# Performance work log

Measured on AMD Instinct MI355X. Metric: run time of the kernel, lower is better.

## Reference

```python
import jax, jax.numpy as jnp
import numpy as np

B, S, V, E, H, L = 32, 64, 96, 256, 512, 3
DIN = 2 * H  # padded input width for stacked LSTM weight tensors


def _cell(x, h, c, Wih, Whh, bih, bhh):
    # PyTorch LSTMCell gate order: i, f, g, o
    g = x @ Wih.T + h @ Whh.T + bih + bhh
    i, f, gg, o = jnp.split(g, 4, axis=-1)
    c2 = jax.nn.sigmoid(f) * c + jax.nn.sigmoid(i) * jnp.tanh(gg)
    h2 = jax.nn.sigmoid(o) * jnp.tanh(c2)
    return h2, c2


def _pad_feat(x, d):
    p = d - x.shape[-1]
    return x if p == 0 else jnp.pad(x, ((0, 0),) * (x.ndim - 1) + ((0, p),))


def _run_lstm(xs, Wih, Whh, bih, bhh, reverse):
    # xs: [S, B, Din]
    if reverse:
        xs = xs[::-1]
    b = xs.shape[1]
    init = (jnp.zeros((b, H), xs.dtype), jnp.zeros((b, H), xs.dtype))

    def step(carry, xt):
        h, c = _cell(xt, carry[0], carry[1], Wih, Whh, bih, bhh)
        return (h, c), h

    (h, c), ys = jax.lax.scan(step, init, xs)
    if reverse:
        ys = ys[::-1]
    return ys, h, c


def setup_inputs():
    key = jax.random.key(0)
    ks = jax.random.split(key, 20)
    f = lambda k, shp, s=0.08: jax.random.normal(k, shp, jnp.float32) * s
    return {
        "src": jax.random.randint(ks[0], (B, S), 0, V - 1),  # avoids padding_idx=95
        "trg": jax.random.randint(ks[1], (B, S), 0, V - 1),
        "embedding": f(ks[2], (V, E), 0.5),
        "enc_Wih": f(ks[3], (L, 2, 4 * H, DIN)),
        "enc_Whh": f(ks[4], (L, 2, 4 * H, H)),
        "enc_bih": f(ks[5], (L, 2, 4 * H)),
        "enc_bhh": f(ks[6], (L, 2, 4 * H)),
        "dec_Wih": f(ks[7], (L, 4 * H, DIN)),
        "dec_Whh": f(ks[8], (L, 4 * H, H)),
        "dec_bih": f(ks[9], (L, 4 * H)),
        "dec_bhh": f(ks[10], (L, 4 * H)),
        "attn_W": f(ks[11], (H, 3 * H)),
        "attn_b": f(ks[12], (H,)),
        "attn_v": jax.random.uniform(ks[13], (H,), jnp.float32),
        "proj_W": f(ks[14], (2 * H, E + 2 * H)),
        "proj_b": f(ks[15], (2 * H,)),
        "fc_W": f(ks[16], (V, H)),
        "fc_b": f(ks[17], (V,)),
    }


def _forward(src, trg, embedding, enc_Wih, enc_Whh, enc_bih, enc_bhh,
             dec_Wih, dec_Whh, dec_bih, dec_bhh, attn_W, attn_b, attn_v,
             proj_W, proj_b, fc_W, fc_b):
    emb = embedding[src]                 # [B,S,E]; dropout=identity (eval)
    xs = emb.transpose(1, 0, 2)          # [S,B,E]
    h_sum, c_sum = [], []
    for l in range(L):
        xin = _pad_feat(xs, DIN)         # zero-pad so stacked weights apply; padded cols hit zeros
        yf, hf, cf = _run_lstm(xin, enc_Wih[l, 0], enc_Whh[l, 0], enc_bih[l, 0], enc_bhh[l, 0], False)
        yb, hb, cb = _run_lstm(xin, enc_Wih[l, 1], enc_Whh[l, 1], enc_bih[l, 1], enc_bhh[l, 1], True)
        xs = jnp.concatenate([yf, yb], -1)  # [S,B,2H]
        h_sum.append(hf + hb)
        c_sum.append(cf + cb)            # hidden.view(L,2,B,H).sum(dim=1)
    enc_out = xs.transpose(1, 0, 2)      # [B,S,2H]
    dec_h, dec_c = jnp.stack(h_sum), jnp.stack(c_sum)  # [L,B,H]

    tokens = trg[:, :-1].T               # teacher_forcing_ratio = 1.0 (deterministic)

    def dec_step(carry, tok):
        h, c = carry
        htop = h[-1]                     # [B,H]
        rep = jnp.concatenate([jnp.broadcast_to(htop[:, None, :], (B, S, H)), enc_out], -1)
        energy = jnp.tanh(rep @ attn_W.T + attn_b)               # [B,S,H]
        attn = jax.nn.softmax(jnp.einsum('d,bsd->bs', attn_v, energy), axis=1)
        context = jnp.einsum('bs,bsd->bd', attn, enc_out)        # [B,2H]
        x = jnp.concatenate([embedding[tok], context], -1) @ proj_W.T + proj_b  # [B,2H]
        hs, cs = [], []
        xin = x
        for l in range(L):
            hl, cl = _cell(_pad_feat(xin, DIN), h[l], c[l], dec_Wih[l], dec_Whh[l], dec_bih[l], dec_bhh[l])
            hs.append(hl)
            cs.append(cl)
            xin = hl
        out = xin @ fc_W.T + fc_b        # [B,V]
        return (jnp.stack(hs), jnp.stack(cs)), out

    _, outs = jax.lax.scan(dec_step, (dec_h, dec_c), tokens)     # [S-1,B,V]
    outputs = jnp.concatenate([jnp.zeros((1, B, V), outs.dtype), outs], 0)
    return outputs.transpose(1, 0, 2)    # [B,S,V]; t=0 row is zeros, matching torch


def reference(src, trg, embedding, enc_Wih, enc_Whh, enc_bih, enc_bhh,
              dec_Wih, dec_Whh, dec_bih, dec_bhh, attn_W, attn_b, attn_v,
              proj_W, proj_b, fc_W, fc_b):
    return _forward(src, trg, embedding, enc_Wih, enc_Whh, enc_bih, enc_bhh,
                    dec_Wih, dec_Whh, dec_bih, dec_bhh, attn_W, attn_b, attn_v,
                    proj_W, proj_b, fc_W, fc_b)
```

## Files before the change

### kernel.cpp

```cpp
#include <hip/hip_runtime.h>

#define B_ 32
#define S_ 64
#define V_ 96
#define E_ 256
#define H_ 512
#define L_ 3
#define DIN_ 1024
#define G4_ 2048
#define BH_ (B_*H_)
#define BDIN_ (B_*DIN_)
#define FSTRIDE 16

typedef unsigned short u16;

__device__ __forceinline__ float bfu(u16 u){ return __uint_as_float(((unsigned)u) << 16); }
__device__ __forceinline__ u16 f2b(float f){
  unsigned x = __float_as_uint(f);
  unsigned r = (x + 0x7FFFu + ((x >> 16) & 1u)) >> 16;
  return (u16)r;
}
__device__ __forceinline__ float sigm(float x){ return 1.f/(1.f+__expf(-x)); }
__device__ __forceinline__ float bsum(float a){
  #pragma unroll
// ... 201 lines not shown
    const int bE = lane & 31;
    const float* Gp = a.G + (size_t)(t*B_+bE)*4096 + (size_t)d*G4_ + j;
    float pg0=Gp[0], pg1=Gp[512], pg2=Gp[1024], pg3=Gp[1536];

    float gv0=0.f, gv1=0.f, gv2=0.f, gv3=0.f;
    for(int b=half*16; b<half*16+16; b++){
      float gs[4] = {0.f,0.f,0.f,0.f};
      const float* hp = &SM[(b<<9) + (lane<<2)];
      #pragma unroll
      for(int pp=0;pp<2;pp++){
        float4 hv = *(const float4*)(hp + pp*256);
        float ha[4] = {hv.x,hv.y,hv.z,hv.w};
        #pragma unroll
        for(int gg=0;gg<4;gg++){
          #pragma unroll
          for(int i=0;i<4;i++) gs[gg] = fmaf(ha[i], wh[gg][pp*4+i], gs[gg]);
        }
      }
      #pragma unroll
      for(int gg=0;gg<4;gg++) gs[gg] = bsum(gs[gg]);
      if(lane == b){ gv0=gs[0]; gv1=gs[1]; gv2=gs[2]; gv3=gs[3]; }
    }
    if(own){
      float gi = gv0+pg0, gf = gv1+pg1, gG = gv2+pg2, go = gv3+pg3;
      float c2 = sigm(gf)*cv + sigm(gi)*tanhf(gG);
      float h2 = sigm(go)*tanhf(c2);
      cv = c2;
      stc(&a.henc[(size_t)(((p+1)&63)*2 + d)*BH_ + (size_t)lane*H_ + j], h2);
      a.Xout[(size_t)(t*B_+lane)*DIN_ + (d<<9) + j] = h2;
    }
    gbar(a.flags, ++g);
  }
  if(own) stc(&a.cT[ci], cv);
  gbar(a.flags, ++g);
  for(int i = blockIdx.x*512 + tid; i < BH_; i += 131072){
    float hf2 = a.henc[(size_t)(0*2+0)*BH_ + i];
    float hb2 = a.henc[(size_t)(0*2+1)*BH_ + i];
    a.dh0[(size_t)a.l*BH_ + i] = hf2 + hb2;
    a.dcT[(size_t)a.l*BH_ + i] = ldc(&a.cT[i]) + ldc(&a.cT[BH_ + i]);
  }
}
__global__ __launch_bounds__(512,1) void k_enc2(EncArgs2 a){
  if(*a.fl) enc2_body<1>(a); else enc2_body<0>(a);
}

struct DecArgs2 {
  const int* trg;
  const void* emb; const void* aW; const void* av; const void* pW; const void* pb;
  const void* dWih; const void* dWhh; const void* dbih; const void* dbhh;
  const void* fW; const void* fb;
  const float* Epre; const float* X3;
  const float* dh0;
  float* dhb;
  float* zb;
  u16*   ctxb;
  float* xpb;
  const float* dcT;
  void* out;
  const int* fl;
  int* flags; int gbase;
};

template<int BF, int CP>
__device__ __forceinline__ void dec2_cell(const DecArgs2& a, float* SM,
    const int t, const int l, const int jp, const int bh, const int bh_blk,
    const int lane, const int tid, const int half, int& g, float& cv){
  constexpr int Kx  = CP*256;
  constexpr int HB  = (CP==4) ? 2 : 1;
  constexpr int NBs = 16/HB;
  constexpr int NW  = NBs/2;
  const float* xsrc = (l==0) ? (a.xpb + (size_t)t*BDIN_ + (size_t)bh_blk*16*DIN_)
                             : (a.dhb + (size_t)((t+1)*3 + (l-1))*BH_ + (size_t)bh_blk*16*H_);
  const float* hsrc = (t==0) ? (a.dh0 + (size_t)l*BH_ + (size_t)bh_blk*16*H_)
                             : (a.dhb + (size_t)(t*3 + l)*BH_ + (size_t)bh_blk*16*H_);
  float wx[4][CP*4];
  float wh[4][8];
  #pragma unroll
  for(int gg=0; gg<4; gg++){
    size_t rowx = ((size_t)l*G4_ + (size_t)gg*H_ + jp)*DIN_;
    #pragma unroll
    for(int p=0;p<CP;p++){
      float4 v = LD4<BF>(a.dWih, rowx + (lane<<2) + p*256);
      wx[gg][p*4+0]=v.x; wx[gg][p*4+1]=v.y; wx[gg][p*4+2]=v.z; wx[gg][p*4+3]=v.w;
    }
    size_t rowh = ((size_t)l*G4_ + (size_t)gg*H_ + jp)*H_;
    #pragma unroll
    for(int p=0;p<2;p++){
      float4 v = LD4<BF>(a.dWhh, rowh + (lane<<2) + p*256);
      wh[gg][p*4+0]=v.x; wh[gg][p*4+1]=v.y; wh[gg][p*4+2]=v.z; wh[gg][p*4+3]=v.w;
    }
  }
  float pg[4];
  {
    size_t bb = (size_t)l*G4_ + jp;
    #pragma unroll
    for(int gg=0;gg<4;gg++)
      pg[gg] = LD<BF>(a.dbih, bb + (size_t)gg*H_) + LD<BF>(a.dbhh, bb + (size_t)gg*H_);
  }
  float gv0=0.f,gv1=0.f,gv2=0.f,gv3=0.f;
  #pragma unroll
  for(int hf=0; hf<HB; hf++){
    const float* xg = xsrc + (size_t)hf*NBs*Kx;
    const float* hg = hsrc + (size_t)hf*NBs*H_;
    for(int i=tid<<2; i<NBs*Kx; i+=2048) *(float4*)&SM[i] = *(const float4*)&xg[i];
    for(int i=tid<<2; i<NBs*H_; i+=2048) *(float4*)&SM[NBs*Kx + i] = *(const float4*)&hg[i];
    __syncthreads();
    for(int ib2=half*NW; ib2<half*NW+NW; ib2++){
      const int ib = hf*NBs + ib2;
      float gs[4] = {0.f,0.f,0.f,0.f};
      const float* xr = &SM[ib2*Kx + (lane<<2)];
      #pragma unroll
      for(int p=0;p<CP;p++){
        float4 xv = *(const float4*)(xr + p*256);
        float xa[4] = {xv.x,xv.y,xv.z,xv.w};
        #pragma unroll
        for(int gg=0;gg<4;gg++){
          #pragma unroll
          for(int i=0;i<4;i++) gs[gg] = fmaf(xa[i], wx[gg][p*4+i], gs[gg]);
        }
      }
      const float* hr = &SM[NBs*Kx + ib2*H_ + (lane<<2)];
      #pragma unroll
      for(int p=0;p<2;p++){
        float4 hv = *(const float4*)(hr + p*256);
        float ha[4] = {hv.x,hv.y,hv.z,hv.w};
        #pragma unroll
        for(int gg=0;gg<4;gg++){
          #pragma unroll
          for(int i=0;i<4;i++) gs[gg] = fmaf(ha[i], wh[gg][p*4+i], gs[gg]);
        }
      }
      #pragma unroll
      for(int gg=0;gg<4;gg++) gs[gg] = bsum(gs[gg]);
      if(lane == ib){ gv0=gs[0]; gv1=gs[1]; gv2=gs[2]; gv3=gs[3]; }
    }
    __syncthreads();
  }
  const bool own = (lane < 16) && (((CP==4) ? ((lane>>2)&1) : (lane>>3)) == half);
  if(own){
    const int b = bh*16 + lane;
    float gi = gv0+pg[0], gf = gv1+pg[1], gG = gv2+pg[2], go = gv3+pg[3];
    float c2 = sigm(gf)*cv + sigm(gi)*tanhf(gG);
    float h2 = sigm(go)*tanhf(c2);
    cv = c2;
    stc(&a.dhb[(size_t)((t+1)*3 + l)*BH_ + (size_t)b*H_ + jp], h2);
  }
  gbar(a.flags, ++g);
}

template<int BF>
__device__ void dec2_body(const DecArgs2& a){
  __shared__ float SM[16384];
  const int tid  = threadIdx.x;
  const int lane = tid & 63;
  const int wid  = tid >> 6;
  const int w4   = (blockIdx.x<<2) + (wid & 3);
  const int jp   = w4 & 511;
  const int bh   = w4 >> 9;
  const int half = wid >> 2;
  const int bh_blk = blockIdx.x >> 7;
  int g = a.gbase;

  float cvs[3];
  #pragma unroll
  for(int l=0;l<3;l++)
    cvs[l] = a.dcT[((size_t)l*H_ + jp)*32 + (size_t)bh*16 + (lane&15)];

  for(int t=0; t<64; ++t){
    {
      const float* hs = (t==0) ? (a.dh0 + (size_t)2*BH_ + (size_t)bh_blk*16*H_)
                               : (a.dhb + (size_t)(t*3 + 2)*BH_ + (size_t)bh_blk*16*H_);
      for(int i=tid<<2; i<16*H_; i+=2048) *(float4*)&SM[i] = *(const float4*)&hs[i];
      __syncthreads();
      if(t < 63){
        float wz[8];
        size_t rz = (size_t)jp*1536;
        #pragma unroll
        for(int p=0;p<2;p++){
          float4 v = LD4<BF>(a.aW, rz + (lane<<2) + p*256);
          wz[p*4+0]=v.x; wz[p*4+1]=v.y; wz[p*4+2]=v.z; wz[p*4+3]=v.w;
        }
        for(int ib=half*8; ib<half*8+8; ib++){
          const float* hp = &SM[(ib<<9) + (lane<<2)];
          float acc = 0.f;
          #pragma unroll
          for(int p=0;p<2;p++){
            float4 hv = *(const float4*)(hp + p*256);
            acc = fmaf(hv.x, wz[p*4+0], acc); acc = fmaf(hv.y, wz[p*4+1], acc);
            acc = fmaf(hv.z, wz[p*4+2], acc); acc = fmaf(hv.w, wz[p*4+3], acc);
          }
          acc = bsum(acc);
          if(lane==0) stc(&a.zb[(size_t)t*BH_ + (size_t)(bh*16+ib)*H_ + jp], acc);
        }
      }
      if(t > 0){
        #pragma unroll
        for(int r=0;r<3;r++){
          const int q  = jp + (r<<9);
          const int v_ = q % 96;
          const int ib = q / 96;
          if((ib>>3) != half) continue;
          float wf[8];
          size_t rf = (size_t)v_*H_;
          #pragma unroll
          for(int p=0;p<2;p++){
            float4 v = LD4<BF>(a.fW, rf + (lane<<2) + p*256);
            wf[p*4+0]=v.x; wf[p*4+1]=v.y; wf[p*4+2]=v.z; wf[p*4+3]=v.w;
          }
          const float* hp = &SM[(ib<<9) + (lane<<2)];
          float acc = 0.f;
          #pragma unroll
          for(int p=0;p<2;p++){
            float4 hv = *(const float4*)(hp + p*256);
            acc = fmaf(hv.x, wf[p*4+0], acc); acc = fmaf(hv.y, wf[p*4+1], acc);
            acc = fmaf(hv.z, wf[p*4+2], acc); acc = fmaf(hv.w, wf[p*4+3], acc);
          }
          acc = bsum(acc);
          if(lane==0){
            float rr = acc + LD<BF>(a.fb, v_);
            size_t oi = (size_t)(bh*16+ib)*(S_*V_) + (size_t)t*V_ + v_;
            if constexpr(BF) ((u16*)a.out)[oi] = f2b(rr);
            else             ((float*)a.out)[oi] = rr;
          }
        }
      }
    }
    if(t == 63) break;
    gbar(a.flags, ++g);

    if(blockIdx.x < 32){
      const int b = blockIdx.x;
      float* Zs = SM; float* Ss = SM + 512;
      for(int i=tid; i<512; i+=512) Zs[i] = a.zb[(size_t)t*BH_ + (size_t)b*H_ + i];
      __syncthreads();
      float wa[8];
      #pragma unroll
      for(int p=0;p<2;p++){
        float4 v = LD4<BF>(a.av, (lane<<2) + p*256);
        wa[p*4+0]=v.x; wa[p*4+1]=v.y; wa[p*4+2]=v.z; wa[p*4+3]=v.w;
      }
      for(int s=wid; s<64; s+=8){
        const float* ep = a.Epre + ((size_t)(s*B_ + b))*H_;
        float acc = 0.f;
        #pragma unroll
        for(int p=0;p<2;p++){
          const float4 e4 = *(const float4*)(ep + (lane<<2) + p*256);
          const float4 z4 = *(const float4*)(Zs + (lane<<2) + p*256);
          acc = fmaf(wa[p*4+0], tanhf(e4.x+z4.x), acc);
          acc = fmaf(wa[p*4+1], tanhf(e4.y+z4.y), acc);
          acc = fmaf(wa[p*4+2], tanhf(e4.z+z4.z), acc);
          acc = fmaf(wa[p*4+3], tanhf(e4.w+z4.w), acc);
        }
        acc = bsum(acc);
        if(lane==0) Ss[s] = acc;
      }
      __syncthreads();
      if(tid < 64){
        float vv = Ss[tid];
        float m = vv;
        #pragma unroll
        for(int off=1; off<64; off<<=1) m = fmaxf(m, __shfl_xor(m, off));
        float e = __expf(vv - m);
        float su = e;
        #pragma unroll
        for(int off=1; off<64; off<<=1) su += __shfl_xor(su, off);
        Ss[tid] = e / su;
      }
      __syncthreads();
      for(int d4 = tid<<2; d4 < DIN_; d4 += 2048){
        float a0=0.f,a1=0.f,a2=0.f,a3=0.f;
        const float* xb = a.X3 + (size_t)b*DIN_ + d4;
        for(int s=0;s<64;s++){
          const float pp = Ss[s];
          const float4 xv = *(const float4*)(xb + (size_t)s*BDIN_);
          a0 = fmaf(pp, xv.x, a0); a1 = fmaf(pp, xv.y, a1);
          a2 = fmaf(pp, xv.z, a2); a3 = fmaf(pp, xv.w, a3);
        }
        u16* cp = a.ctxb + (size_t)t*BDIN_ + (size_t)b*DIN_ + d4;
        unsigned lo = (unsigned)f2b(a0) | ((unsigned)f2b(a1)<<16);
        unsigned hi = (unsigned)f2b(a2) | ((unsigned)f2b(a3)<<16);
        stci((int*)cp, (int)lo);
        stci(((int*)cp)+1, (int)hi);
      }
    }
    gbar(a.flags, ++g);

    {
      const u16* cs = a.ctxb + (size_t)t*BDIN_ + (size_t)bh_blk*16*DIN_;
      for(int i=tid*4; i<16*DIN_; i+=2048){
        ushort4 v = *(const ushort4*)(cs + i);
        *(float4*)&SM[i] = make_float4(bfu(v.x), bfu(v.y), bfu(v.z), bfu(v.w));
      }
      __syncthreads();
      float wpe[2][4], wpc[2][16];
      #pragma unroll
      for(int jj=0;jj<2;jj++){
        size_t row = (size_t)(jp + (jj<<9))*1280;
        float4 v = LD4<BF>(a.pW, row + (lane<<2));
        wpe[jj][0]=v.x; wpe[jj][1]=v.y; wpe[jj][2]=v.z; wpe[jj][3]=v.w;
        #pragma unroll
        for(int p=0;p<4;p++){
          float4 c4 = LD4<BF>(a.pW, row + 256 + (lane<<2) + p*256);
          wpc[jj][p*4+0]=c4.x; wpc[jj][p*4+1]=c4.y; wpc[jj][p*4+2]=c4.z; wpc[jj][p*4+3]=c4.w;
        }
      }
      const float pb0 = LD<BF>(a.pb, jp);
      const float pb1 = LD<BF>(a.pb, jp+512);
      for(int ib=half*8; ib<half*8+8; ib++){
        const int b = bh*16 + ib;
        const int tok = a.trg[b*S_ + t];
        float4 ev = LD4<BF>(a.emb, (size_t)tok*E_ + (lane<<2));
        float ea[4] = {ev.x, ev.y, ev.z, ev.w};
        float s0=0.f, s1=0.f;
        #pragma unroll
        for(int i=0;i<4;i++){ s0 = fmaf(ea[i], wpe[0][i], s0); s1 = fmaf(ea[i], wpe[1][i], s1); }
        const float* cp = &SM[(ib<<10) + (lane<<2)];
        #pragma unroll
        for(int p=0;p<4;p++){
          float4 c4 = *(const float4*)(cp + p*256);
          float ca[4] = {c4.x,c4.y,c4.z,c4.w};
          #pragma unroll
          for(int i=0;i<4;i++){ s0 = fmaf(ca[i], wpc[0][p*4+i], s0); s1 = fmaf(ca[i], wpc[1][p*4+i], s1); }
        }
        s0 = bsum(s0); s1 = bsum(s1);
        if(lane==0){
          stc(&a.xpb[(size_t)t*BDIN_ + (size_t)b*DIN_ + jp],       s0 + pb0);
          stc(&a.xpb[(size_t)t*BDIN_ + (size_t)b*DIN_ + jp + 512], s1 + pb1);
        }
      }
      __syncthreads();
    }
    gbar(a.flags, ++g);

    dec2_cell<BF,4>(a, SM, t, 0, jp, bh, bh_blk, lane, tid, half, g, cvs[0]);
    dec2_cell<BF,2>(a, SM, t, 1, jp, bh, bh_blk, lane, tid, half, g, cvs[1]);
    dec2_cell<BF,2>(a, SM, t, 2, jp, bh, bh_blk, lane, tid, half, g, cvs[2]);
  }
}
__global__ __launch_bounds__(512,1) void k_dec2(DecArgs2 a){
  if(*a.fl) dec2_body<1>(a); else dec2_body<0>(a);
}

struct EncArgsO {
  const float* G;
  const float* Xin;
  const void* Wih; size_t oWi;
  const void* Whh; size_t oWh;
  const void* bih; size_t obi;
  const void* bhh; size_t obh;
  float* hst; float* cT; float* Xout; float* dh; float* dcT;
  int l; const int* fl; int* flags; int gbase;
};

template<int BF, int CP>
__device__ void encO_body(const EncArgsO& a){
  __shared__ float SM[16384];
  const int tid  = threadIdx.x;
  const int w    = (blockIdx.x<<2) + (tid>>6);
  const int lane = tid & 63;
  const int d    = w >> 9;
  const int j    = w & 511;
  int g = a.gbase;

  float wh[4][8];
  #pragma unroll
  for(int gg=0; gg<4; gg++){
    size_t rowh = a.oWh + ((size_t)d*G4_ + (size_t)gg*H_ + j)*H_;
    #pragma unroll
    for(int p=0;p<2;p++){
      float4 v = LD4<BF>(a.Whh, rowh + (lane<<2) + p*256);
      wh[gg][p*4+0]=v.x; wh[gg][p*4+1]=v.y; wh[gg][p*4+2]=v.z; wh[gg][p*4+3]=v.w;
    }
  }
  float wxf[4][CP?CP*4:1];
  float pbias[4];
  if constexpr(CP>0){
    #pragma unroll
    for(int gg=0; gg<4; gg++){
      size_t rowx = a.oWi + ((size_t)d*G4_ + (size_t)gg*H_ + j)*DIN_;
      #pragma unroll
      for(int p=0;p<CP;p++){
        float4 v = LD4<BF>(a.Wih, rowx + (lane<<2) + p*256);
        wxf[gg][p*4+0]=v.x; wxf[gg][p*4+1]=v.y; wxf[gg][p*4+2]=v.z; wxf[gg][p*4+3]=v.w;
      }
    }
    size_t bb = (size_t)d*G4_ + j;
    #pragma unroll
    for(int gg=0;gg<4;gg++)
      pbias[gg] = LD<BF>(a.bih, a.obi + bb + (size_t)gg*H_)
// ... 345 lines not shown
          stc(&a.xp[(size_t)b*DIN_ + jp + 512], s1 + pb1);
        }
      }
    }
    gbar(a.flags, ++g);
    decO_cell<BF,4>(a, SM, 0, cur, jp, bh, bh_blk, lane, tid, g, cvs[0]);
    decO_cell<BF,2>(a, SM, 1, cur, jp, bh, bh_blk, lane, tid, g, cvs[1]);
    decO_cell<BF,2>(a, SM, 2, cur, jp, bh, bh_blk, lane, tid, g, cvs[2]);
    cur ^= 1;
  }
}
__global__ __launch_bounds__(256,2) void k_dec_persO(DecArgsO a){
  if(*a.fl) decO_body<1>(a); else decO_body<0>(a);
}

extern "C" void kernel_launch(void* const* d_in, const int* in_sizes, int n_in,
                              void* d_out, int out_size, void* d_ws, size_t ws_size,
                              hipStream_t stream){
  const int* src  = (const int*)d_in[0];
  const int* trg  = (const int*)d_in[1];
  const void* emb = d_in[2];
  const void* eWih= d_in[3];
  const void* eWhh= d_in[4];
  const void* ebih= d_in[5];
  const void* ebhh= d_in[6];
  const void* dWih= d_in[7];
  const void* dWhh= d_in[8];
  const void* dbih= d_in[9];
  const void* dbhh= d_in[10];
  const void* aW  = d_in[11];
  const void* ab  = d_in[12];
  const void* av  = d_in[13];
  const void* pW  = d_in[14];
  const void* pb  = d_in[15];
  const void* fW  = d_in[16];
  const void* fb  = d_in[17];

  char* base = (char*)d_ws;
  size_t off = 0;
  auto take = [&](size_t bytes)->char*{
    char* p = base + off; off = (off + bytes + 255) & ~(size_t)255; return p;
  };

  const size_t szX  = (size_t)2048*1024*4;
  const size_t szG  = (size_t)2048*4096*4;
  const size_t szE  = (size_t)2048*512*4;
  int planA = ws_size >= (size_t)53*1024*1024;

  if(planA){
    float* X    = (float*)take(szX);
    float* Xh   = (float*)take(szX);
    float* G    = (float*)take(szG);
    float* dhb  = G;
    float* zb   = dhb + (size_t)64*3*BH_;
    float* xpb  = zb  + (size_t)63*BH_;
    u16*   ctxb = (u16*)(xpb + (size_t)63*BDIN_);
    float* Epre = (float*)take(szE);
    float* cTe  = (float*)take((size_t)2*BH_*4);
    float* dh0  = (float*)take((size_t)3*BH_*4);
    float* dcT  = (float*)take((size_t)3*BH_*4);
    int* fl     = (int*)take(256);
    int* flags  = (int*)take((256*FSTRIDE + 16)*4);

    k_detect<<<1, 256, 0, stream>>>(av, fl, flags);
    k_embed<<<8192, 256, 0, stream>>>(src, emb, X, fl);

    for(int l=0;l<L_;l++){
      int K = (l==0) ? E_ : DIN_;
      k_gemm<<<dim3(64,16), 256, 0, stream>>>(X, DIN_,
          eWih, DIN_, (size_t)l*2*G4_*DIN_,
          ebih, (size_t)l*2*G4_, ebhh, (size_t)l*2*G4_,
          G, 4096, K, fl);
      EncArgs2 ea;
      ea.G = G; ea.Whh = eWhh; ea.oWh = (size_t)l*2*G4_*H_;
      ea.henc = Xh; ea.cT = cTe; ea.Xout = X;
      ea.dh0 = dh0; ea.dcT = dcT; ea.l = l;
      ea.fl = fl; ea.flags = flags; ea.gbase = l*65;
      k_enc2<<<256, 512, 0, stream>>>(ea);
    }
    k_gemm<<<dim3(8,16), 256, 0, stream>>>(X, DIN_,
        aW, 3*H_, (size_t)H_, ab, 0, nullptr, 0, Epre, H_, DIN_, fl);
    k_outzero<<<12, 256, 0, stream>>>(d_out, fl);

    DecArgs2 da;
    da.trg = trg; da.emb = emb; da.aW = aW; da.av = av; da.pW = pW; da.pb = pb;
    da.dWih = dWih; da.dWhh = dWhh; da.dbih = dbih; da.dbhh = dbhh;
    da.fW = fW; da.fb = fb;
    da.Epre = Epre; da.X3 = X;
    da.dh0 = dh0; da.dhb = dhb; da.zb = zb; da.ctxb = ctxb; da.xpb = xpb;
    da.dcT = dcT; da.out = d_out; da.fl = fl; da.flags = flags; da.gbase = 3*65;
    k_dec2<<<256, 512, 0, stream>>>(da);
  } else {
    float* XA   = (float*)take(szX);
    float* XB   = (float*)take(szX);
    float* Epre = (float*)take(szE);
    float* hst  = (float*)take((size_t)4*BH_*4);
    float* cTe  = (float*)take((size_t)2*BH_*4);
    float* dh   = (float*)take((size_t)6*BH_*4);
    float* dcT  = (float*)take((size_t)3*BH_*4);
    float* zbuf = (float*)take((size_t)BH_*4);
    float* ctx  = (float*)take((size_t)2*BH_*4);
    float* xp   = (float*)take((size_t)2*BH_*4);
    int* fl     = (int*)take(256);
    int* flags  = (int*)take((256*FSTRIDE + 16)*4);

    k_detect<<<1, 256, 0, stream>>>(av, fl, flags);
    k_embed<<<8192, 256, 0, stream>>>(src, emb, XA, fl);

    float* Xin = XA; float* Xout = XB;
    for(int l=0;l<L_;l++){
      EncArgsO ea;
      ea.G = nullptr; ea.Xin = Xin;
      ea.Wih = eWih; ea.oWi = (size_t)l*2*G4_*DIN_;
      ea.Whh = eWhh; ea.oWh = (size_t)l*2*G4_*H_;
      ea.bih = ebih; ea.obi = (size_t)l*2*G4_;
      ea.bhh = ebhh; ea.obh = (size_t)l*2*G4_;
      ea.hst = hst; ea.cT = cTe; ea.Xout = Xout;
      ea.dh = dh; ea.dcT = dcT; ea.l = l;
      ea.fl = fl; ea.flags = flags; ea.gbase = l*65;
      if(l == 0) k_enc_persF0<<<256, 256, 0, stream>>>(ea);
      else       k_enc_persF12<<<256, 256, 0, stream>>>(ea);
      float* tmp = Xin; Xin = Xout; Xout = tmp;
    }
    k_gemm<<<dim3(8,16), 256, 0, stream>>>(Xin, DIN_,
        aW, 3*H_, (size_t)H_, ab, 0, nullptr, 0, Epre, H_, DIN_, fl);
    k_outzero<<<12, 256, 0, stream>>>(d_out, fl);

    DecArgsO da;
    da.trg = trg; da.emb = emb; da.aW = aW; da.av = av; da.pW = pW; da.pb = pb;
    da.dWih = dWih; da.dWhh = dWhh; da.dbih = dbih; da.dbhh = dbhh;
    da.fW = fW; da.fb = fb;
    da.Epre = Epre; da.X3 = Xin;
    da.dh = dh; da.dcT = dcT; da.z = zbuf; da.ctx = ctx; da.xp = xp;
    da.out = d_out; da.fl = fl; da.flags = flags; da.gbase = 3*65;
    k_dec_persO<<<256, 256, 0, stream>>>(da);
  }
}
```

Measured before the change: 10.47 ms.

## Fuse decoder attention/projection into per-batch blocks and cut grid barriers per step

Restructures the persistent decoder kernel. Blocks 0-31 now each handle one batch row and compute the fc output, attention query, softmax, context and input projection locally. This removes two grid-wide barriers per timestep, along with the zb and ctxb global scratch buffers. LSTM cells are now split so each wave owns 8 batch rows for one hidden unit, and the next layer's weights are prefetched before each barrier. The trade-off is that the attention and projection work, including full weight-row streams per thread, is serialized onto 32 blocks, which may lengthen the critical path.

```diff
diff --git a/kernel.cpp b/kernel.cpp
--- a/kernel.cpp
+++ b/kernel.cpp
@@ -277,8 +277,6 @@
   const float* Epre; const float* X3;
   const float* dh0;
   float* dhb;
-  float* zb;
-  u16*   ctxb;
   float* xpb;
   const float* dcT;
   void* out;
@@ -287,19 +285,8 @@
 };
 
 template<int BF, int CP>
-__device__ __forceinline__ void dec2_cell(const DecArgs2& a, float* SM,
-    const int t, const int l, const int jp, const int bh, const int bh_blk,
-    const int lane, const int tid, const int half, int& g, float& cv){
-  constexpr int Kx  = CP*256;
-  constexpr int HB  = (CP==4) ? 2 : 1;
-  constexpr int NBs = 16/HB;
-  constexpr int NW  = NBs/2;
-  const float* xsrc = (l==0) ? (a.xpb + (size_t)t*BDIN_ + (size_t)bh_blk*16*DIN_)
-                             : (a.dhb + (size_t)((t+1)*3 + (l-1))*BH_ + (size_t)bh_blk*16*H_);
-  const float* hsrc = (t==0) ? (a.dh0 + (size_t)l*BH_ + (size_t)bh_blk*16*H_)
-                             : (a.dhb + (size_t)(t*3 + l)*BH_ + (size_t)bh_blk*16*H_);
-  float wx[4][CP*4];
-  float wh[4][8];
+__device__ __forceinline__ void dec_loadW(const DecArgs2& a, const int l,
+    const int jp, const int lane, float wx[4][16], float wh[4][8], float pg[4]){
   #pragma unroll
   for(int gg=0; gg<4; gg++){
     size_t rowx = ((size_t)l*G4_ + (size_t)gg*H_ + jp)*DIN_;
@@ -315,251 +302,211 @@
       wh[gg][p*4+0]=v.x; wh[gg][p*4+1]=v.y; wh[gg][p*4+2]=v.z; wh[gg][p*4+3]=v.w;
     }
   }
-  float pg[4];
-  {
-    size_t bb = (size_t)l*G4_ + jp;
-    #pragma unroll
-    for(int gg=0;gg<4;gg++)
-      pg[gg] = LD<BF>(a.dbih, bb + (size_t)gg*H_) + LD<BF>(a.dbhh, bb + (size_t)gg*H_);
-  }
+  size_t bb = (size_t)l*G4_ + jp;
+  #pragma unroll
+  for(int gg=0;gg<4;gg++)
+    pg[gg] = LD<BF>(a.dbih, bb + (size_t)gg*H_) + LD<BF>(a.dbhh, bb + (size_t)gg*H_);
+}
+
+template<int BF, int CP>
+__device__ __forceinline__ void dec_cellc(const DecArgs2& a, float* SM,
+    const int t, const int l, const int jp, const int bq,
+    const int lane, const int tid,
+    float wx[4][16], float wh[4][8], float pg[4], float& cv){
+  constexpr int Kx = CP*256;
+  const float* xsrc = (l==0) ? (a.xpb + (size_t)t*BDIN_ + (size_t)bq*8*DIN_)
+                             : (a.dhb + (size_t)((t+1)*3 + (l-1))*BH_ + (size_t)bq*8*H_);
+  const float* hsrc = (t==0) ? (a.dh0 + (size_t)l*BH_ + (size_t)bq*8*H_)
+                             : (a.dhb + (size_t)(t*3 + l)*BH_ + (size_t)bq*8*H_);
+  for(int i=tid<<2; i<8*Kx; i+=2048) *(float4*)&SM[i] = *(const float4*)&xsrc[i];
+  for(int i=tid<<2; i<8*H_; i+=2048) *(float4*)&SM[8*Kx + i] = *(const float4*)&hsrc[i];
+  __syncthreads();
   float gv0=0.f,gv1=0.f,gv2=0.f,gv3=0.f;
-  #pragma unroll
-  for(int hf=0; hf<HB; hf++){
-    const float* xg = xsrc + (size_t)hf*NBs*Kx;
-    const float* hg = hsrc + (size_t)hf*NBs*H_;
-    for(int i=tid<<2; i<NBs*Kx; i+=2048) *(float4*)&SM[i] = *(const float4*)&xg[i];
-    for(int i=tid<<2; i<NBs*H_; i+=2048) *(float4*)&SM[NBs*Kx + i] = *(const float4*)&hg[i];
-    __syncthreads();
-    for(int ib2=half*NW; ib2<half*NW+NW; ib2++){
-      const int ib = hf*NBs + ib2;
-      float gs[4] = {0.f,0.f,0.f,0.f};
-      const float* xr = &SM[ib2*Kx + (lane<<2)];
-      #pragma unroll
-      for(int p=0;p<CP;p++){
-        float4 xv = *(const float4*)(xr + p*256);
-        float xa[4] = {xv.x,xv.y,xv.z,xv.w};
-        #pragma unroll
-        for(int gg=0;gg<4;gg++){
-          #pragma unroll
-          for(int i=0;i<4;i++) gs[gg] = fmaf(xa[i], wx[gg][p*4+i], gs[gg]);
-        }
-      }
-      const float* hr = &SM[NBs*Kx + ib2*H_ + (lane<<2)];
-      #pragma unroll
-      for(int p=0;p<2;p++){
-        float4 hv = *(const float4*)(hr + p*256);
-        float ha[4] = {hv.x,hv.y,hv.z,hv.w};
-        #pragma unroll
-        for(int gg=0;gg<4;gg++){
-          #pragma unroll
-          for(int i=0;i<4;i++) gs[gg] = fmaf(ha[i], wh[gg][p*4+i], gs[gg]);
-        }
-      }
-      #pragma unroll
-      for(int gg=0;gg<4;gg++) gs[gg] = bsum(gs[gg]);
-      if(lane == ib){ gv0=gs[0]; gv1=gs[1]; gv2=gs[2]; gv3=gs[3]; }
-    }
-    __syncthreads();
-  }
-  const bool own = (lane < 16) && (((CP==4) ? ((lane>>2)&1) : (lane>>3)) == half);
-  if(own){
-    const int b = bh*16 + lane;
+  for(int ib=0; ib<8; ib++){
+    float gs[4] = {0.f,0.f,0.f,0.f};
+    const float* xr = &SM[ib*Kx + (lane<<2)];
+    #pragma unroll
+    for(int p=0;p<CP;p++){
+      float4 xv = *(const float4*)(xr + p*256);
+      float xa[4] = {xv.x,xv.y,xv.z,xv.w};
+      #pragma unroll
+      for(int gg=0;gg<4;gg++){
+        #pragma unroll
+        for(int i=0;i<4;i++) gs[gg] = fmaf(xa[i], wx[gg][p*4+i], gs[gg]);
+      }
+    }
+    const float* hr = &SM[8*Kx + ib*H_ + (lane<<2)];
+    #pragma unroll
+    for(int p=0;p<2;p++){
+      float4 hv = *(const float4*)(hr + p*256);
+      float ha[4] = {hv.x,hv.y,hv.z,hv.w};
+      #pragma unroll
+      for(int gg=0;gg<4;gg++){
+        #pragma unroll
+        for(int i=0;i<4;i++) gs[gg] = fmaf(ha[i], wh[gg][p*4+i], gs[gg]);
+      }
+    }
+    #pragma unroll
+    for(int gg=0;gg<4;gg++) gs[gg] = bsum(gs[gg]);
+    if(lane == ib){ gv0=gs[0]; gv1=gs[1]; gv2=gs[2]; gv3=gs[3]; }
+  }
+  if(lane < 8){
+    const int b = bq*8 + lane;
     float gi = gv0+pg[0], gf = gv1+pg[1], gG = gv2+pg[2], go = gv3+pg[3];
     float c2 = sigm(gf)*cv + sigm(gi)*tanhf(gG);
     float h2 = sigm(go)*tanhf(c2);
     cv = c2;
     stc(&a.dhb[(size_t)((t+1)*3 + l)*BH_ + (size_t)b*H_ + jp], h2);
   }
-  gbar(a.flags, ++g);
 }
 
 template<int BF>
 __device__ void dec2_body(const DecArgs2& a){
-  __shared__ float SM[16384];
+  __shared__ float SM[12288];
   const int tid  = threadIdx.x;
   const int lane = tid & 63;
   const int wid  = tid >> 6;
-  const int w4   = (blockIdx.x<<2) + (wid & 3);
-  const int jp   = w4 & 511;
-  const int bh   = w4 >> 9;
-  const int half = wid >> 2;
-  const int bh_blk = blockIdx.x >> 7;
+  const int w8   = (blockIdx.x<<3) + wid;
+  const int jp   = w8 & 511;
+  const int bq   = w8 >> 9;
   int g = a.gbase;
 
   float cvs[3];
   #pragma unroll
   for(int l=0;l<3;l++)
-    cvs[l] = a.dcT[((size_t)l*H_ + jp)*32 + (size_t)bh*16 + (lane&15)];
+    cvs[l] = a.dcT[((size_t)l*H_ + jp)*32 + (size_t)bq*8 + (lane&7)];
+
+  float wx[4][16], wh[4][8], pg[4];
 
   for(int t=0; t<64; ++t){
-    {
-      const float* hs = (t==0) ? (a.dh0 + (size_t)2*BH_ + (size_t)bh_blk*16*H_)
-                               : (a.dhb + (size_t)(t*3 + 2)*BH_ + (size_t)bh_blk*16*H_);
-      for(int i=tid<<2; i<16*H_; i+=2048) *(float4*)&SM[i] = *(const float4*)&hs[i];
-      __syncthreads();
-      if(t < 63){
-        float wz[8];
-        size_t rz = (size_t)jp*1536;
-        #pragma unroll
-        for(int p=0;p<2;p++){
-          float4 v = LD4<BF>(a.aW, rz + (lane<<2) + p*256);
-          wz[p*4+0]=v.x; wz[p*4+1]=v.y; wz[p*4+2]=v.z; wz[p*4+3]=v.w;
-        }
-        for(int ib=half*8; ib<half*8+8; ib++){
-          const float* hp = &SM[(ib<<9) + (lane<<2)];
-          float acc = 0.f;
-          #pragma unroll
-          for(int p=0;p<2;p++){
-            float4 hv = *(const float4*)(hp + p*256);
-            acc = fmaf(hv.x, wz[p*4+0], acc); acc = fmaf(hv.y, wz[p*4+1], acc);
-            acc = fmaf(hv.z, wz[p*4+2], acc); acc = fmaf(hv.w, wz[p*4+3], acc);
-          }
-          acc = bsum(acc);
-          if(lane==0) stc(&a.zb[(size_t)t*BH_ + (size_t)(bh*16+ib)*H_ + jp], acc);
-        }
-      }
-      if(t > 0){
-        #pragma unroll
-        for(int r=0;r<3;r++){
-          const int q  = jp + (r<<9);
-          const int v_ = q % 96;
-          const int ib = q / 96;
-          if((ib>>3) != half) continue;
-          float wf[8];
-          size_t rf = (size_t)v_*H_;
-          #pragma unroll
-          for(int p=0;p<2;p++){
-            float4 v = LD4<BF>(a.fW, rf + (lane<<2) + p*256);
-            wf[p*4+0]=v.x; wf[p*4+1]=v.y; wf[p*4+2]=v.z; wf[p*4+3]=v.w;
-          }
-          const float* hp = &SM[(ib<<9) + (lane<<2)];
-          float acc = 0.f;
-          #pragma unroll
-          for(int p=0;p<2;p++){
-            float4 hv = *(const float4*)(hp + p*256);
-            acc = fmaf(hv.x, wf[p*4+0], acc); acc = fmaf(hv.y, wf[p*4+1], acc);
-            acc = fmaf(hv.z, wf[p*4+2], acc); acc = fmaf(hv.w, wf[p*4+3], acc);
-          }
-          acc = bsum(acc);
-          if(lane==0){
-            float rr = acc + LD<BF>(a.fb, v_);
-            size_t oi = (size_t)(bh*16+ib)*(S_*V_) + (size_t)t*V_ + v_;
-            if constexpr(BF) ((u16*)a.out)[oi] = f2b(rr);
-            else             ((float*)a.out)[oi] = rr;
-          }
-        }
-      }
-    }
-    if(t == 63) break;
-    gbar(a.flags, ++g);
-
     if(blockIdx.x < 32){
       const int b = blockIdx.x;
-      float* Zs = SM; float* Ss = SM + 512;
-      for(int i=tid; i<512; i+=512) Zs[i] = a.zb[(size_t)t*BH_ + (size_t)b*H_ + i];
+      float* Ht = SM;
+      float* Zs = SM + 512;
+      float* Cx = SM + 1024;
+      float* Ss = SM + 2048;
+      float* Em = SM + 2176;
+      const float* hs = (t==0) ? (a.dh0 + (size_t)2*BH_ + (size_t)b*H_)
+                               : (a.dhb + (size_t)(t*3 + 2)*BH_ + (size_t)b*H_);
+      Ht[tid] = hs[tid];
       __syncthreads();
-      float wa[8];
-      #pragma unroll
-      for(int p=0;p<2;p++){
-        float4 v = LD4<BF>(a.av, (lane<<2) + p*256);
-        wa[p*4+0]=v.x; wa[p*4+1]=v.y; wa[p*4+2]=v.z; wa[p*4+3]=v.w;
-      }
-      for(int s=wid; s<64; s+=8){
-        const float* ep = a.Epre + ((size_t)(s*B_ + b))*H_;
+      if(t > 0 && tid < 96){
         float acc = 0.f;
-        #pragma unroll
-        for(int p=0;p<2;p++){
-          const float4 e4 = *(const float4*)(ep + (lane<<2) + p*256);
-          const float4 z4 = *(const float4*)(Zs + (lane<<2) + p*256);
-          acc = fmaf(wa[p*4+0], tanhf(e4.x+z4.x), acc);
-          acc = fmaf(wa[p*4+1], tanhf(e4.y+z4.y), acc);
-          acc = fmaf(wa[p*4+2], tanhf(e4.z+z4.z), acc);
-          acc = fmaf(wa[p*4+3], tanhf(e4.w+z4.w), acc);
-        }
-        acc = bsum(acc);
-        if(lane==0) Ss[s] = acc;
-      }
-      __syncthreads();
-      if(tid < 64){
-        float vv = Ss[tid];
-        float m = vv;
-        #pragma unroll
-        for(int off=1; off<64; off<<=1) m = fmaxf(m, __shfl_xor(m, off));
-        float e = __expf(vv - m);
-        float su = e;
-        #pragma unroll
-        for(int off=1; off<64; off<<=1) su += __shfl_xor(su, off);
-        Ss[tid] = e / su;
-      }
-      __syncthreads();
-      for(int d4 = tid<<2; d4 < DIN_; d4 += 2048){
-        float a0=0.f,a1=0.f,a2=0.f,a3=0.f;
-        const float* xb = a.X3 + (size_t)b*DIN_ + d4;
-        for(int s=0;s<64;s++){
-          const float pp = Ss[s];
-          const float4 xv = *(const float4*)(xb + (size_t)s*BDIN_);
-          a0 = fmaf(pp, xv.x, a0); a1 = fmaf(pp, xv.y, a1);
-          a2 = fmaf(pp, xv.z, a2); a3 = fmaf(pp, xv.w, a3);
-        }
-        u16* cp = a.ctxb + (size_t)t*BDIN_ + (size_t)b*DIN_ + d4;
-        unsigned lo = (unsigned)f2b(a0) | ((unsigned)f2b(a1)<<16);
-        unsigned hi = (unsigned)f2b(a2) | ((unsigned)f2b(a3)<<16);
-        stci((int*)cp, (int)lo);
-        stci(((int*)cp)+1, (int)hi);
-      }
-    }
+        size_t rf = (size_t)tid*H_;
+        #pragma unroll 4
+        for(int k=0;k<H_;k+=4){
+          float4 wv = LD4<BF>(a.fW, rf + k);
+          acc = fmaf(Ht[k],wv.x,acc); acc = fmaf(Ht[k+1],wv.y,acc);
+          acc = fmaf(Ht[k+2],wv.z,acc); acc = fmaf(Ht[k+3],wv.w,acc);
+        }
+        float rr = acc + LD<BF>(a.fb, tid);
+        size_t oi = (size_t)b*(S_*V_) + (size_t)t*V_ + tid;
+        if constexpr(BF) ((u16*)a.out)[oi] = f2b(rr);
+        else             ((float*)a.out)[oi] = rr;
+      }
+      if(t < 63){
+        {
+          float acc = 0.f;
+          size_t rz = (size_t)tid*1536;
+          #pragma unroll 4
+          for(int k=0;k<512;k+=4){
+            float4 wv = LD4<BF>(a.aW, rz + k);
+            acc = fmaf(Ht[k],wv.x,acc); acc = fmaf(Ht[k+1],wv.y,acc);
+            acc = fmaf(Ht[k+2],wv.z,acc); acc = fmaf(Ht[k+3],wv.w,acc);
+          }
+          Zs[tid] = acc;
+        }
+        __syncthreads();
+        {
+          float wa[8];
+          #pragma unroll
+          for(int p=0;p<2;p++){
+            float4 v = LD4<BF>(a.av, (lane<<2) + p*256);
+            wa[p*4+0]=v.x; wa[p*4+1]=v.y; wa[p*4+2]=v.z; wa[p*4+3]=v.w;
+          }
+          for(int s=wid*8; s<wid*8+8; s++){
+            const float* ep = a.Epre + ((size_t)(s*B_ + b))*H_;
+            float acc = 0.f;
+            #pragma unroll
+            for(int p=0;p<2;p++){
+              const float4 e4 = *(const float4*)(ep + (lane<<2) + p*256);
+              const float4 z4 = *(const float4*)(Zs + (lane<<2) + p*256);
+              acc = fmaf(wa[p*4+0], tanhf(e4.x+z4.x), acc);
+              acc = fmaf(wa[p*4+1], tanhf(e4.y+z4.y), acc);
+              acc = fmaf(wa[p*4+2], tanhf(e4.z+z4.z), acc);
+              acc = fmaf(wa[p*4+3], tanhf(e4.w+z4.w), acc);
+            }
+            acc = bsum(acc);
+            if(lane==0) Ss[s] = acc;
+          }
+        }
+        __syncthreads();
+        if(tid < 64){
+          float vv = Ss[tid];
+          float m = vv;
+          #pragma unroll
+          for(int off=1; off<64; off<<=1) m = fmaxf(m, __shfl_xor(m, off));
+          float e = __expf(vv - m);
+          float su = e;
+          #pragma unroll
+          for(int off=1; off<64; off<<=1) su += __shfl_xor(su, off);
+          Ss[tid] = e / su;
+        }
+        __syncthreads();
+        if(tid < 256){
+          int d4 = tid<<2;
+          float a0=0.f,a1=0.f,a2=0.f,a3=0.f;
+          const float* xb = a.X3 + (size_t)b*DIN_ + d4;
+          #pragma unroll 4
+          for(int s=0;s<64;s++){
+            const float pp = Ss[s];
+            const float4 xv = *(const float4*)(xb + (size_t)s*BDIN_);
+            a0 = fmaf(pp, xv.x, a0); a1 = fmaf(pp, xv.y, a1);
+            a2 = fmaf(pp, xv.z, a2); a3 = fmaf(pp, xv.w, a3);
+          }
+          *(float4*)&Cx[d4] = make_float4(a0,a1,a2,a3);
+        }
+        if(tid < 64){
+          int tok = a.trg[b*S_ + t];
+          float4 ev = LD4<BF>(a.emb, (size_t)tok*E_ + (tid<<2));
+          *(float4*)&Em[tid<<2] = ev;
+        }
+        __syncthreads();
+        {
+          #pragma unroll
+          for(int jj=0;jj<2;jj++){
+            const int j = tid + (jj<<9);
+            size_t row = (size_t)j*1280;
+            float acc = 0.f;
+            #pragma unroll 4
+            for(int k=0;k<256;k+=4){
+              float4 wv = LD4<BF>(a.pW, row + k);
+              acc = fmaf(Em[k],wv.x,acc); acc = fmaf(Em[k+1],wv.y,acc);
+              acc = fmaf(Em[k+2],wv.z,acc); acc = fmaf(Em[k+3],wv.w,acc);
+            }
+            #pragma unroll 4
+            for(int k=0;k<1024;k+=4){
+              float4 wv = LD4<BF>(a.pW, row + 256 + k);
+              acc = fmaf(Cx[k],wv.x,acc); acc = fmaf(Cx[k+1],wv.y,acc);
+              acc = fmaf(Cx[k+2],wv.z,acc); acc = fmaf(Cx[k+3],wv.w,acc);
+            }
+            stc(&a.xpb[(size_t)t*BDIN_ + (size_t)b*DIN_ + j], acc + LD<BF>(a.pb, j));
+          }
+        }
+      }
+    }
+    if(t == 63) break;
+
+    dec_loadW<BF,4>(a, 0, jp, lane, wx, wh, pg);
     gbar(a.flags, ++g);
-
-    {
-      const u16* cs = a.ctxb + (size_t)t*BDIN_ + (size_t)bh_blk*16*DIN_;
-      for(int i=tid*4; i<16*DIN_; i+=2048){
-        ushort4 v = *(const ushort4*)(cs + i);
-        *(float4*)&SM[i] = make_float4(bfu(v.x), bfu(v.y), bfu(v.z), bfu(v.w));
-      }
-      __syncthreads();
-      float wpe[2][4], wpc[2][16];
-      #pragma unroll
-      for(int jj=0;jj<2;jj++){
-        size_t row = (size_t)(jp + (jj<<9))*1280;
-        float4 v = LD4<BF>(a.pW, row + (lane<<2));
-        wpe[jj][0]=v.x; wpe[jj][1]=v.y; wpe[jj][2]=v.z; wpe[jj][3]=v.w;
-        #pragma unroll
-        for(int p=0;p<4;p++){
-          float4 c4 = LD4<BF>(a.pW, row + 256 + (lane<<2) + p*256);
-          wpc[jj][p*4+0]=c4.x; wpc[jj][p*4+1]=c4.y; wpc[jj][p*4+2]=c4.z; wpc[jj][p*4+3]=c4.w;
-        }
-      }
-      const float pb0 = LD<BF>(a.pb, jp);
-      const float pb1 = LD<BF>(a.pb, jp+512);
-      for(int ib=half*8; ib<half*8+8; ib++){
-        const int b = bh*16 + ib;
-        const int tok = a.trg[b*S_ + t];
-        float4 ev = LD4<BF>(a.emb, (size_t)tok*E_ + (lane<<2));
-        float ea[4] = {ev.x, ev.y, ev.z, ev.w};
-        float s0=0.f, s1=0.f;
-        #pragma unroll
-        for(int i=0;i<4;i++){ s0 = fmaf(ea[i], wpe[0][i], s0); s1 = fmaf(ea[i], wpe[1][i], s1); }
-        const float* cp = &SM[(ib<<10) + (lane<<2)];
-        #pragma unroll
-        for(int p=0;p<4;p++){
-          float4 c4 = *(const float4*)(cp + p*256);
-          float ca[4] = {c4.x,c4.y,c4.z,c4.w};
-          #pragma unroll
-          for(int i=0;i<4;i++){ s0 = fmaf(ca[i], wpc[0][p*4+i], s0); s1 = fmaf(ca[i], wpc[1][p*4+i], s1); }
-        }
-        s0 = bsum(s0); s1 = bsum(s1);
-        if(lane==0){
-          stc(&a.xpb[(size_t)t*BDIN_ + (size_t)b*DIN_ + jp],       s0 + pb0);
-          stc(&a.xpb[(size_t)t*BDIN_ + (size_t)b*DIN_ + jp + 512], s1 + pb1);
-        }
-      }
-      __syncthreads();
-    }
+    dec_cellc<BF,4>(a, SM, t, 0, jp, bq, lane, tid, wx, wh, pg, cvs[0]);
+    dec_loadW<BF,2>(a, 1, jp, lane, wx, wh, pg);
     gbar(a.flags, ++g);
-
-    dec2_cell<BF,4>(a, SM, t, 0, jp, bh, bh_blk, lane, tid, half, g, cvs[0]);
-    dec2_cell<BF,2>(a, SM, t, 1, jp, bh, bh_blk, lane, tid, half, g, cvs[1]);
-    dec2_cell<BF,2>(a, SM, t, 2, jp, bh, bh_blk, lane, tid, half, g, cvs[2]);
+    dec_cellc<BF,2>(a, SM, t, 1, jp, bq, lane, tid, wx, wh, pg, cvs[1]);
+    dec_loadW<BF,2>(a, 2, jp, lane, wx, wh, pg);
+    gbar(a.flags, ++g);
+    dec_cellc<BF,2>(a, SM, t, 2, jp, bq, lane, tid, wx, wh, pg, cvs[2]);
+    gbar(a.flags, ++g);
   }
 }
 __global__ __launch_bounds__(512,1) void k_dec2(DecArgs2 a){
@@ -1011,9 +958,7 @@
     float* Xh   = (float*)take(szX);
     float* G    = (float*)take(szG);
     float* dhb  = G;
-    float* zb   = dhb + (size_t)64*3*BH_;
-    float* xpb  = zb  + (size_t)63*BH_;
-    u16*   ctxb = (u16*)(xpb + (size_t)63*BDIN_);
+    float* xpb  = dhb + (size_t)64*3*BH_;
     float* Epre = (float*)take(szE);
     float* cTe  = (float*)take((size_t)2*BH_*4);
     float* dh0  = (float*)take((size_t)3*BH_*4);
@@ -1046,7 +991,7 @@
     da.dWih = dWih; da.dWhh = dWhh; da.dbih = dbih; da.dbhh = dbhh;
     da.fW = fW; da.fb = fb;
     da.Epre = Epre; da.X3 = X;
-    da.dh0 = dh0; da.dhb = dhb; da.zb = zb; da.ctxb = ctxb; da.xpb = xpb;
+    da.dh0 = dh0; da.dhb = dhb; da.xpb = xpb;
     da.dcT = dcT; da.out = d_out; da.fl = fl; da.flags = flags; da.gbase = 3*65;
     k_dec2<<<256, 512, 0, stream>>>(da);
   } else {
```

After: 20.45 ms. 1.95x slower.

## Split decoder LSTM gates across wave halves and prefetch weights before grid barriers

Applied to the files above, without the earlier changes.

Work in the decoder cell is now split by gate instead of by batch rows. Each half of the block computes two of the four gates for all 16 batch rows, and the halves combine their partial gate values through shared memory before the cell update. Weight and bias loads for the next layer are issued before the grid barrier, so their latency can overlap the barrier wait. Each thread now holds fewer weight registers, which lowers register pressure. In exchange it adds an extra shared-memory exchange and a block sync per layer, and each wave now iterates over all 16 batch rows.

```diff
diff --git a/kernel.cpp b/kernel.cpp
--- a/kernel.cpp
+++ b/kernel.cpp
@@ -287,42 +287,42 @@
 };
 
 template<int BF, int CP>
-__device__ __forceinline__ void dec2_cell(const DecArgs2& a, float* SM,
+__device__ __forceinline__ void dec_loadW(const DecArgs2& a, const int l,
+    const int jp, const int lane, const int half,
+    float wx[2][16], float wh[2][8], float pg[2]){
+  #pragma unroll
+  for(int gg=0; gg<2; gg++){
+    const int gr = half*2 + gg;
+    size_t rowx = ((size_t)l*G4_ + (size_t)gr*H_ + jp)*DIN_;
+    #pragma unroll
+    for(int p=0;p<CP;p++){
+      float4 v = LD4<BF>(a.dWih, rowx + (lane<<2) + p*256);
+      wx[gg][p*4+0]=v.x; wx[gg][p*4+1]=v.y; wx[gg][p*4+2]=v.z; wx[gg][p*4+3]=v.w;
+    }
+    size_t rowh = ((size_t)l*G4_ + (size_t)gr*H_ + jp)*H_;
+    #pragma unroll
+    for(int p=0;p<2;p++){
+      float4 v = LD4<BF>(a.dWhh, rowh + (lane<<2) + p*256);
+      wh[gg][p*4+0]=v.x; wh[gg][p*4+1]=v.y; wh[gg][p*4+2]=v.z; wh[gg][p*4+3]=v.w;
+    }
+    size_t bb = (size_t)l*G4_ + (size_t)gr*H_ + jp;
+    pg[gg] = LD<BF>(a.dbih, bb) + LD<BF>(a.dbhh, bb);
+  }
+}
+
+template<int BF, int CP>
+__device__ __forceinline__ void dec_cellG(const DecArgs2& a, float* SM,
     const int t, const int l, const int jp, const int bh, const int bh_blk,
-    const int lane, const int tid, const int half, int& g, float& cv){
+    const int lane, const int tid, const int half, const int pairid,
+    float wx[2][16], float wh[2][8], float pg[2], float& cv){
   constexpr int Kx  = CP*256;
   constexpr int HB  = (CP==4) ? 2 : 1;
   constexpr int NBs = 16/HB;
-  constexpr int NW  = NBs/2;
   const float* xsrc = (l==0) ? (a.xpb + (size_t)t*BDIN_ + (size_t)bh_blk*16*DIN_)
                              : (a.dhb + (size_t)((t+1)*3 + (l-1))*BH_ + (size_t)bh_blk*16*H_);
   const float* hsrc = (t==0) ? (a.dh0 + (size_t)l*BH_ + (size_t)bh_blk*16*H_)
                              : (a.dhb + (size_t)(t*3 + l)*BH_ + (size_t)bh_blk*16*H_);
-  float wx[4][CP*4];
-  float wh[4][8];
-  #pragma unroll
-  for(int gg=0; gg<4; gg++){
-    size_t rowx = ((size_t)l*G4_ + (size_t)gg*H_ + jp)*DIN_;
-    #pragma unroll
-    for(int p=0;p<CP;p++){
-      float4 v = LD4<BF>(a.dWih, rowx + (lane<<2) + p*256);
-      wx[gg][p*4+0]=v.x; wx[gg][p*4+1]=v.y; wx[gg][p*4+2]=v.z; wx[gg][p*4+3]=v.w;
-    }
-    size_t rowh = ((size_t)l*G4_ + (size_t)gg*H_ + jp)*H_;
-    #pragma unroll
-    for(int p=0;p<2;p++){
-      float4 v = LD4<BF>(a.dWhh, rowh + (lane<<2) + p*256);
-      wh[gg][p*4+0]=v.x; wh[gg][p*4+1]=v.y; wh[gg][p*4+2]=v.z; wh[gg][p*4+3]=v.w;
-    }
-  }
-  float pg[4];
-  {
-    size_t bb = (size_t)l*G4_ + jp;
-    #pragma unroll
-    for(int gg=0;gg<4;gg++)
-      pg[gg] = LD<BF>(a.dbih, bb + (size_t)gg*H_) + LD<BF>(a.dbhh, bb + (size_t)gg*H_);
-  }
-  float gv0=0.f,gv1=0.f,gv2=0.f,gv3=0.f;
+  float gvA=0.f, gvB=0.f;
   #pragma unroll
   for(int hf=0; hf<HB; hf++){
     const float* xg = xsrc + (size_t)hf*NBs*Kx;
@@ -330,47 +330,49 @@
     for(int i=tid<<2; i<NBs*Kx; i+=2048) *(float4*)&SM[i] = *(const float4*)&xg[i];
     for(int i=tid<<2; i<NBs*H_; i+=2048) *(float4*)&SM[NBs*Kx + i] = *(const float4*)&hg[i];
     __syncthreads();
-    for(int ib2=half*NW; ib2<half*NW+NW; ib2++){
+    for(int ib2=0; ib2<NBs; ib2++){
       const int ib = hf*NBs + ib2;
-      float gs[4] = {0.f,0.f,0.f,0.f};
+      float gs0=0.f, gs1=0.f;
       const float* xr = &SM[ib2*Kx + (lane<<2)];
       #pragma unroll
       for(int p=0;p<CP;p++){
         float4 xv = *(const float4*)(xr + p*256);
-        float xa[4] = {xv.x,xv.y,xv.z,xv.w};
-        #pragma unroll
-        for(int gg=0;gg<4;gg++){
-          #pragma unroll
-          for(int i=0;i<4;i++) gs[gg] = fmaf(xa[i], wx[gg][p*4+i], gs[gg]);
-        }
+        gs0 = fmaf(xv.x, wx[0][p*4+0], gs0); gs0 = fmaf(xv.y, wx[0][p*4+1], gs0);
+        gs0 = fmaf(xv.z, wx[0][p*4+2], gs0); gs0 = fmaf(xv.w, wx[0][p*4+3], gs0);
+        gs1 = fmaf(xv.x, wx[1][p*4+0], gs1); gs1 = fmaf(xv.y, wx[1][p*4+1], gs1);
+        gs1 = fmaf(xv.z, wx[1][p*4+2], gs1); gs1 = fmaf(xv.w, wx[1][p*4+3], gs1);
       }
       const float* hr = &SM[NBs*Kx + ib2*H_ + (lane<<2)];
       #pragma unroll
       for(int p=0;p<2;p++){
         float4 hv = *(const float4*)(hr + p*256);
-        float ha[4] = {hv.x,hv.y,hv.z,hv.w};
-        #pragma unroll
-        for(int gg=0;gg<4;gg++){
-          #pragma unroll
-          for(int i=0;i<4;i++) gs[gg] = fmaf(ha[i], wh[gg][p*4+i], gs[gg]);
-        }
-      }
-      #pragma unroll
-      for(int gg=0;gg<4;gg++) gs[gg] = bsum(gs[gg]);
-      if(lane == ib){ gv0=gs[0]; gv1=gs[1]; gv2=gs[2]; gv3=gs[3]; }
+        gs0 = fmaf(hv.x, wh[0][p*4+0], gs0); gs0 = fmaf(hv.y, wh[0][p*4+1], gs0);
+        gs0 = fmaf(hv.z, wh[0][p*4+2], gs0); gs0 = fmaf(hv.w, wh[0][p*4+3], gs0);
+        gs1 = fmaf(hv.x, wh[1][p*4+0], gs1); gs1 = fmaf(hv.y, wh[1][p*4+1], gs1);
+        gs1 = fmaf(hv.z, wh[1][p*4+2], gs1); gs1 = fmaf(hv.w, wh[1][p*4+3], gs1);
+      }
+      gs0 = bsum(gs0); gs1 = bsum(gs1);
+      if(lane == ib){ gvA=gs0; gvB=gs1; }
     }
     __syncthreads();
   }
-  const bool own = (lane < 16) && (((CP==4) ? ((lane>>2)&1) : (lane>>3)) == half);
-  if(own){
+  float* comb = SM + 15360 + pairid*128;
+  if(lane < 16){
+    comb[half*32 + lane*2 + 0] = gvA + pg[0];
+    comb[half*32 + lane*2 + 1] = gvB + pg[1];
+  }
+  __syncthreads();
+  if(half == 0 && lane < 16){
     const int b = bh*16 + lane;
-    float gi = gv0+pg[0], gf = gv1+pg[1], gG = gv2+pg[2], go = gv3+pg[3];
+    float gi = comb[lane*2 + 0];
+    float gf = comb[lane*2 + 1];
+    float gG = comb[32 + lane*2 + 0];
+    float go = comb[32 + lane*2 + 1];
     float c2 = sigm(gf)*cv + sigm(gi)*tanhf(gG);
     float h2 = sigm(go)*tanhf(c2);
     cv = c2;
     stc(&a.dhb[(size_t)((t+1)*3 + l)*BH_ + (size_t)b*H_ + jp], h2);
   }
-  gbar(a.flags, ++g);
 }
 
 template<int BF>
@@ -383,6 +385,7 @@
   const int jp   = w4 & 511;
   const int bh   = w4 >> 9;
   const int half = wid >> 2;
+  const int pairid = wid & 3;
   const int bh_blk = blockIdx.x >> 7;
   int g = a.gbase;
 
@@ -390,6 +393,8 @@
   #pragma unroll
   for(int l=0;l<3;l++)
     cvs[l] = a.dcT[((size_t)l*H_ + jp)*32 + (size_t)bh*16 + (lane&15)];
+
+  float wx[2][16], wh[2][8], pg[2];
 
   for(int t=0; t<64; ++t){
     {
@@ -555,11 +560,16 @@
       }
       __syncthreads();
     }
+    dec_loadW<BF,4>(a, 0, jp, lane, half, wx, wh, pg);
     gbar(a.flags, ++g);
-
-    dec2_cell<BF,4>(a, SM, t, 0, jp, bh, bh_blk, lane, tid, half, g, cvs[0]);
-    dec2_cell<BF,2>(a, SM, t, 1, jp, bh, bh_blk, lane, tid, half, g, cvs[1]);
-    dec2_cell<BF,2>(a, SM, t, 2, jp, bh, bh_blk, lane, tid, half, g, cvs[2]);
+    dec_cellG<BF,4>(a, SM, t, 0, jp, bh, bh_blk, lane, tid, half, pairid, wx, wh, pg, cvs[0]);
+    dec_loadW<BF,2>(a, 1, jp, lane, half, wx, wh, pg);
+    gbar(a.flags, ++g);
+    dec_cellG<BF,2>(a, SM, t, 1, jp, bh, bh_blk, lane, tid, half, pairid, wx, wh, pg, cvs[1]);
+    dec_loadW<BF,2>(a, 2, jp, lane, half, wx, wh, pg);
+    gbar(a.flags, ++g);
+    dec_cellG<BF,2>(a, SM, t, 2, jp, bh, bh_blk, lane, tid, half, pairid, wx, wh, pg, cvs[2]);
+    gbar(a.flags, ++g);
   }
 }
 __global__ __launch_bounds__(512,1) void k_dec2(DecArgs2 a){
```

Result: faster. 9.584 ms (-8.4%).
